# Optimization experiments

Hardware: AMD Instinct MI355X
Metric: run time of the kernel (lower is better)

The kernel has to match this reference:

```python
import jax, jax.numpy as jnp
import numpy as np

E_DIM = 64
N_EMBED = 8192

def setup_inputs() -> dict:
    key = jax.random.key(0)
    k1, k2 = jax.random.split(key)
    x = jax.random.normal(k1, (16, E_DIM, 32, 32), dtype=jnp.float32)   # [B, e_dim, H, W]
    embed = jax.random.normal(k2, (E_DIM, N_EMBED), dtype=jnp.float32)  # codebook [e_dim, n_embed]
    return {"x": x, "embed": embed}

def reference(x, embed):
    e_dim, n_embed = embed.shape
    # NCHW -> NHWC
    xp = jnp.transpose(x, (0, 2, 3, 1))              # [B, H, W, e_dim]
    flat = xp.reshape(-1, e_dim)                     # [N, e_dim]
    # squared-distance expansion: ||f||^2 - 2 f.E + ||e||^2  -> [N, n_embed]
    distance = (jnp.sum(flat * flat, axis=1, keepdims=True)
                - 2.0 * flat @ embed
                + jnp.sum(embed * embed, axis=0, keepdims=True))
    embed_idx = jnp.argmax(-distance, axis=1)        # [N] nearest code ids
    embed_idx = embed_idx.reshape(xp.shape[:-1])     # [B, H, W]
    # gather codes: embedding table is embed.T -> [n_embed, e_dim]
    quantize = jnp.take(embed.T, embed_idx, axis=0)  # [B, H, W, e_dim]
    return quantize
```

## Files before the change

kernel.cpp:

```cpp
#include <hip/hip_runtime.h>


typedef __attribute__((ext_vector_type(8))) __bf16 bf16x8;
typedef __attribute__((ext_vector_type(4))) float f32x4;
typedef unsigned int u32;
typedef unsigned long long u64;

union frag_cast { f32x4 f; bf16x8 b; };
__device__ __forceinline__ bf16x8 as_bf16x8(f32x4 v) { frag_cast u; u.f = v; return u.b; }

#define N_ROWS  16384
#define E_DIM   64
#define N_EMBED 8192
#define NCHUNK  16
#define COLS_PER_BLOCK (N_EMBED / NCHUNK)
#define N_ST (COLS_PER_BLOCK / 64)
#define ROWS_PER_BLOCK 512
#define N_ROWBLK (N_ROWS / ROWS_PER_BLOCK)
#define NT 8
#define MARGIN_THR 2e-3f

#define WS_AH   0u
#define WS_AL   (2u << 20)
#define WS_B    (4u << 20)
#define WS_ET   (6u << 20)
#define WS_BIAS (8u << 20)
#define WS_CNT  (WS_BIAS + (32u << 10))
#define WS_PB1  (WS_CNT + (4u << 10))
#define WS_PI1  (WS_PB1 + (1u << 20))
#define WS_PB2  (WS_PI1 + (1u << 20))

__device__ __forceinline__ u32 f32_key(float s) {
    u32 u = __float_as_uint(s);
    return (u & 0x80000000u) ? ~u : (u | 0x80000000u);
}

__device__ __forceinline__ void async16(const void* g, void* l) {
    __builtin_amdgcn_global_load_lds(
        (const __attribute__((address_space(1))) void*)g,
        (__attribute__((address_space(3))) void*)l, 16, 0, 0);
}

__global__ __launch_bounds__(256) void prep(
        const float* __restrict__ x, const float* __restrict__ embed, char* ws) {
    __shared__ float tile[64][65];
    __bf16* Ah = (__bf16*)(ws + WS_AH);
    __bf16* Al = (__bf16*)(ws + WS_AL);
    float*  eT = (float*)(ws + WS_ET);
    float*  bias = (float*)(ws + WS_BIAS);
    const int t = threadIdx.x;
    const int blk = blockIdx.x;

    if (blk < 256) {
        const int b = blk >> 4, p0 = (blk & 15) * 64;
        {
            const int c = t >> 2, seg = (t & 3) * 16;
            const float* src = x + b * 65536 + c * 1024 + p0 + seg;
#pragma unroll
            for (int i = 0; i < 16; ++i) tile[c][seg + i] = src[i];
        }
        __syncthreads();
        const int p = t >> 2, cq = (t & 3) * 16;
        const long row = b * 1024 + p0 + p;
        bf16x8 vh0, vh1, vl0, vl1;
#pragma unroll
        for (int i = 0; i < 16; ++i) {
            float f = tile[cq + i][p];
            __bf16 h = (__bf16)f;
            __bf16 l = (__bf16)(f - (float)h);
            if (i < 8) { vh0[i] = h; vl0[i] = l; }
            else       { vh1[i - 8] = h; vl1[i - 8] = l; }
        }
        *(bf16x8*)(Ah + row * 64 + cq) = vh0;
        *(bf16x8*)(Ah + row * 64 + cq + 8) = vh1;
        *(bf16x8*)(Al + row * 64 + cq) = vl0;
        *(bf16x8*)(Al + row * 64 + cq + 8) = vl1;
    } else {
        const int g = blk - 256;
        const int jbase = g * 64;
        char* Bg = ws + WS_B + (size_t)g * 16384;
        {
            const int c = t >> 2, seg = (t & 3) * 16;
            const float* src = embed + c * N_EMBED + jbase + seg;
#pragma unroll
            for (int i = 0; i < 16; ++i) tile[c][seg + i] = src[i];
        }
        __syncthreads();
        if (t < 64) {
            float s = 0.f;
#pragma unroll
            for (int c = 0; c < 64; ++c) { float v = tile[c][t]; s = fmaf(v, v, s); }
            bias[jbase + t] = -0.5f * s;
        }
        const int jl = t >> 2, cq = (t & 3) * 16;
        bf16x8 vh0, vh1, vl0, vl1;
#pragma unroll
        for (int i = 0; i < 16; ++i) {
            float f = tile[cq + i][jl];
            eT[(long)(jbase + jl) * 64 + cq + i] = f;
            __bf16 h = (__bf16)f;
            __bf16 l = (__bf16)(f - (float)h);
            if (i < 8) { vh0[i] = h; vl0[i] = l; }
            else       { vh1[i - 8] = h; vl1[i - 8] = l; }
        }
        const int k0 = (cq >> 3), sw = jl & 7;
        __bf16* hi = (__bf16*)Bg + jl * 64;
        __bf16* lo = (__bf16*)(Bg + 8192) + jl * 64;
        *(bf16x8*)(hi + ((k0 ^ sw) * 8))       = vh0;
        *(bf16x8*)(hi + (((k0 + 1) ^ sw) * 8)) = vh1;
        *(bf16x8*)(lo + ((k0 ^ sw) * 8))       = vl0;
        *(bf16x8*)(lo + (((k0 + 1) ^ sw) * 8)) = vl1;
    }
}

__global__ __launch_bounds__(256, 2) void qdist(const char* __restrict__ ws_c, char* __restrict__ ws) {
    __shared__ __align__(16) char smem[2][16384];
    const __bf16* Ah = (const __bf16*)(ws_c + WS_AH);
    const __bf16* Al = (const __bf16*)(ws_c + WS_AL);
    const char* Bws = ws_c + WS_B;
    const float* biasg = (const float*)(ws_c + WS_BIAS);
    float* pb1 = (float*)(ws + WS_PB1);
    int*   pi1 = (int*)(ws + WS_PI1);
    float* pb2 = (float*)(ws + WS_PB2);

    const int t = threadIdx.x;
    const int wv = t >> 6, lane = t & 63, ln = lane & 15, q = lane >> 4;
    const int rb = blockIdx.x >> 4, chunk = blockIdx.x & 15;
    const int row0 = rb * ROWS_PER_BLOCK;
    const int col0 = chunk * COLS_PER_BLOCK;
    const int g0 = col0 >> 6;

    f32x4 pfh[NT][2], pfl[NT][2];
#pragma unroll
    for (int nt = 0; nt < NT; ++nt) {
        long row = row0 + wv * 128 + nt * 16 + ln;
        long base = row * 64 + q * 8;
        pfh[nt][0] = *(const f32x4*)(Ah + base);
        pfh[nt][1] = *(const f32x4*)(Ah + base + 32);
        pfl[nt][0] = *(const f32x4*)(Al + base);
        pfl[nt][1] = *(const f32x4*)(Al + base + 32);
    }
    asm volatile("" :
        "+v"(pfh[0][0]), "+v"(pfh[0][1]), "+v"(pfh[1][0]), "+v"(pfh[1][1]),
        "+v"(pfh[2][0]), "+v"(pfh[2][1]), "+v"(pfh[3][0]), "+v"(pfh[3][1]),
        "+v"(pfh[4][0]), "+v"(pfh[4][1]), "+v"(pfh[5][0]), "+v"(pfh[5][1]),
        "+v"(pfh[6][0]), "+v"(pfh[6][1]), "+v"(pfh[7][0]), "+v"(pfh[7][1]));
    asm volatile("" :
        "+v"(pfl[0][0]), "+v"(pfl[0][1]), "+v"(pfl[1][0]), "+v"(pfl[1][1]),
        "+v"(pfl[2][0]), "+v"(pfl[2][1]), "+v"(pfl[3][0]), "+v"(pfl[3][1]),
        "+v"(pfl[4][0]), "+v"(pfl[4][1]), "+v"(pfl[5][0]), "+v"(pfl[5][1]),
        "+v"(pfl[6][0]), "+v"(pfl[6][1]), "+v"(pfl[7][0]), "+v"(pfl[7][1]));

    float b1[NT], b2[NT]; int iq[NT];
#pragma unroll
    for (int k = 0; k < NT; ++k) { b1[k] = -3.4e38f; b2[k] = -3.4e38f; iq[k] = 0; }

    const int s7 = ln & 7;
    const int rdbase = ln * 128 + ((q ^ s7) << 4);

    auto issue = [&](int st) {
        const char* src = Bws + (size_t)(g0 + st) * 16384;
        char* dst = smem[st & 1];
#pragma unroll
        for (int s = 0; s < 4; ++s)
            async16(src + s * 4096 + wv * 1024 + lane * 16,
                    dst + s * 4096 + wv * 1024);
    };

    issue(0);
    for (int st = 0; st < N_ST; ++st) {
        __syncthreads();
        if (st + 1 < N_ST) issue(st + 1);
        const char* buf = smem[st & 1];
        __builtin_amdgcn_s_setprio(1);
#pragma unroll
        for (int ct = 0; ct < 4; ++ct) {
            const int boff = ct * 2048 + rdbase;
            bf16x8 ah0 = *(const bf16x8*)(buf + boff);
            bf16x8 ah1 = *(const bf16x8*)(buf + (boff ^ 64));
            bf16x8 al0 = *(const bf16x8*)(buf + 8192 + boff);
            bf16x8 al1 = *(const bf16x8*)(buf + 8192 + (boff ^ 64));
            const int cbase = col0 + st * 64 + ct * 16;
            f32x4 bv = *(const f32x4*)(biasg + cbase + q * 4);
            const int jq = cbase + q * 4;
#pragma unroll
            for (int nt = 0; nt < NT; ++nt) {
                f32x4 acc = __builtin_amdgcn_mfma_f32_16x16x32_bf16(al0, as_bf16x8(pfh[nt][0]), bv, 0, 0, 0);
                acc = __builtin_amdgcn_mfma_f32_16x16x32_bf16(al1, as_bf16x8(pfh[nt][1]), acc, 0, 0, 0);
                acc = __builtin_amdgcn_mfma_f32_16x16x32_bf16(ah0, as_bf16x8(pfl[nt][0]), acc, 0, 0, 0);
                acc = __builtin_amdgcn_mfma_f32_16x16x32_bf16(ah1, as_bf16x8(pfl[nt][1]), acc, 0, 0, 0);
                acc = __builtin_amdgcn_mfma_f32_16x16x32_bf16(ah0, as_bf16x8(pfh[nt][0]), acc, 0, 0, 0);
                acc = __builtin_amdgcn_mfma_f32_16x16x32_bf16(ah1, as_bf16x8(pfh[nt][1]), acc, 0, 0, 0);
                float mx = fmaxf(fmaxf(acc[0], acc[1]), fmaxf(acc[2], acc[3]));
                b2[nt] = fmaxf(b2[nt], fminf(b1[nt], mx));
                bool gt = mx > b1[nt];
                b1[nt] = fmaxf(b1[nt], mx);
                iq[nt] = gt ? jq : iq[nt];
            }
        }
        __builtin_amdgcn_s_setprio(0);
    }

#pragma unroll
    for (int m = 16; m < 64; m <<= 1) {
#pragma unroll
        for (int nt = 0; nt < NT; ++nt) {
            float o1 = __shfl_xor(b1[nt], m);
            int   oi = __shfl_xor(iq[nt], m);
            float o2 = __shfl_xor(b2[nt], m);
            b2[nt] = fmaxf(fmaxf(fminf(b1[nt], o1), o2), b2[nt]);
            bool take = (o1 > b1[nt]) || (o1 == b1[nt] && oi < iq[nt]);
            if (take) { b1[nt] = o1; iq[nt] = oi; }
        }
    }
    if (q == 0) {
#pragma unroll
        for (int nt = 0; nt < NT; ++nt) {
            int pixel = row0 + wv * 128 + nt * 16 + ln;
            int o = chunk * N_ROWS + pixel;
            pb1[o] = b1[nt];
            pi1[o] = iq[nt];
            pb2[o] = b2[nt];
        }
    }
}

__global__ __launch_bounds__(256) void reduce_rows(const float* __restrict__ x, char* ws,
                                                   float* __restrict__ out) {
    const float* pb1 = (const float*)(ws + WS_PB1);
    const int*   pi1 = (const int*)(ws + WS_PI1);
    const float* pb2 = (const float*)(ws + WS_PB2);
    const float* eT = (const float*)(ws + WS_ET);
    const float* bias = (const float*)(ws + WS_BIAS);
    const int t = threadIdx.x;
    const int lane = t & 63, wv = t >> 6;
    const int row = (blockIdx.x * 256 + t) >> 2;
    const int sub = t & 3;

    float m1 = -3.4e38f, m2 = -3.4e38f; int mi = 0;
#pragma unroll
    for (int k = 0; k < 4; ++k) {
        const int ch = sub * 4 + k;
        float o1 = pb1[ch * N_ROWS + row];
        int   oi = pi1[ch * N_ROWS + row];
        float o2 = pb2[ch * N_ROWS + row];
        m2 = fmaxf(fmaxf(fminf(m1, o1), o2), m2);
        if (o1 > m1 || (o1 == m1 && oi < mi)) { m1 = o1; mi = oi; }
    }
#pragma unroll
    for (int m = 1; m < 4; m <<= 1) {
        float o1 = __shfl_xor(m1, m);
        int   oi = __shfl_xor(mi, m);
        float o2 = __shfl_xor(m2, m);
        m2 = fmaxf(fmaxf(fminf(m1, o1), o2), m2);
        bool take = (o1 > m1) || (o1 == m1 && oi < mi);
        if (take) { m1 = o1; mi = oi; }
    }

    const bool flagged = (m1 - m2 < MARGIN_THR);
    if (!flagged) {
        const float* xb = x + (row >> 10) * 65536 + (row & 1023);
        const int j = mi + sub;
        const f32x4* ecd = (const f32x4*)(eT + (size_t)j * 64);
        float s = bias[j];
#pragma unroll
        for (int v = 0; v < 16; ++v) {
            f32x4 ev = ecd[v];
            s = fmaf(xb[(v * 4 + 0) * 1024], ev[0], s);
            s = fmaf(xb[(v * 4 + 1) * 1024], ev[1], s);
            s = fmaf(xb[(v * 4 + 2) * 1024], ev[2], s);
            s = fmaf(xb[(v * 4 + 3) * 1024], ev[3], s);
        }
        float best = s; int bj = j;
#pragma unroll
        for (int m = 1; m < 4; m <<= 1) {
            float os = __shfl_xor(best, m);
            int   oj = __shfl_xor(bj, m);
            bool take = (os > best) || (os == best && oj < bj);
            if (take) { best = os; bj = oj; }
        }
        const f32x4* src = (const f32x4*)(eT + (size_t)bj * 64);
        f32x4* dst = (f32x4*)(out + (size_t)row * 64);
#pragma unroll
        for (int v = 0; v < 4; ++v) dst[v * 4 + sub] = src[v * 4 + sub];
    }

    u64 bal = __ballot(flagged);
    const int wrow0 = blockIdx.x * 64 + wv * 16;
    while (bal) {
        const int b = __ffsll(bal) - 1;
        const int rw = b >> 2;
        bal &= ~(0xFull << (rw * 4));
        const int r = wrow0 + rw;
        const float rb1 = __shfl(m1, rw * 4);
        const float cutoff = rb1 - 2.0f * MARGIN_THR;

        float xv = x[(r >> 10) * 65536 + lane * 1024 + (r & 1023)];
        float xr[64];
#pragma unroll
        for (int c = 0; c < 64; ++c) xr[c] = __shfl(xv, c);

        u64 bestk = 0ull;
        for (int ch = 0; ch < NCHUNK; ++ch) {
            if (pb1[ch * N_ROWS + r] < cutoff) continue;
#pragma unroll
            for (int k = 0; k < 8; ++k) {
                const int j = ch * 512 + lane * 8 + k;
                const f32x4* ecd = (const f32x4*)(eT + (size_t)j * 64);
                f32x4 a0 = {0.f, 0.f, 0.f, 0.f}, a1 = a0, a2 = a0, a3 = a0;
#pragma unroll
                for (int v = 0; v < 4; ++v) {
                    f32x4 e0 = ecd[v * 4 + 0], e1 = ecd[v * 4 + 1];
                    f32x4 e2 = ecd[v * 4 + 2], e3 = ecd[v * 4 + 3];
#pragma unroll
                    for (int kk = 0; kk < 4; ++kk) {
                        a0[kk] = fmaf(xr[v * 16 + kk],      e0[kk], a0[kk]);
                        a1[kk] = fmaf(xr[v * 16 + 4 + kk],  e1[kk], a1[kk]);
                        a2[kk] = fmaf(xr[v * 16 + 8 + kk],  e2[kk], a2[kk]);
                        a3[kk] = fmaf(xr[v * 16 + 12 + kk], e3[kk], a3[kk]);
                    }
                }
                f32x4 a01 = a0 + a1, a23 = a2 + a3;
                f32x4 as = a01 + a23;
                float s = bias[j] + ((as[0] + as[1]) + (as[2] + as[3]));
                u64 key = ((u64)f32_key(s) << 32) | (u32)(~(u32)j);
                bestk = (key > bestk) ? key : bestk;
            }
        }
#pragma unroll
        for (int m = 1; m < 64; m <<= 1) {
            u64 o = __shfl_xor(bestk, m);
            bestk = (o > bestk) ? o : bestk;
        }
        const int idx = (int)(~(u32)(bestk & 0xffffffffull));
        out[(size_t)r * 64 + lane] = eT[(size_t)idx * 64 + lane];
    }
}

extern "C" void kernel_launch(void* const* d_in, const int* in_sizes, int n_in,
                              void* d_out, int out_size, void* d_ws, size_t ws_size,
                              hipStream_t stream) {
    const float* x     = (const float*)d_in[0];
    const float* embed = (const float*)d_in[1];
    float* out = (float*)d_out;
    char* ws = (char*)d_ws;

    prep<<<384, 256, 0, stream>>>(x, embed, ws);
    qdist<<<N_ROWBLK * NCHUNK, 256, 0, stream>>>(ws, ws);
    reduce_rows<<<256, 256, 0, stream>>>(x, ws, out);
}
```

Before: 130.2 us.

## Switch distance GEMM to single-pass fp16 with norm-based rigorous rescoring margin

```diff
diff --git a/kernel.cpp b/kernel.cpp
--- a/kernel.cpp
+++ b/kernel.cpp
@@ -1,13 +1,11 @@
 #include <hip/hip_runtime.h>
 
 
-typedef __attribute__((ext_vector_type(8))) __bf16 bf16x8;
+typedef _Float16 f16;
+typedef __attribute__((ext_vector_type(8))) _Float16 f16x8;
 typedef __attribute__((ext_vector_type(4))) float f32x4;
 typedef unsigned int u32;
 typedef unsigned long long u64;
-
-union frag_cast { f32x4 f; bf16x8 b; };
-__device__ __forceinline__ bf16x8 as_bf16x8(f32x4 v) { frag_cast u; u.f = v; return u.b; }
 
 #define N_ROWS  16384
 #define E_DIM   64
@@ -18,17 +16,16 @@
 #define ROWS_PER_BLOCK 512
 #define N_ROWBLK (N_ROWS / ROWS_PER_BLOCK)
 #define NT 8
-#define MARGIN_THR 2e-3f
 
 #define WS_AH   0u
-#define WS_AL   (2u << 20)
-#define WS_B    (4u << 20)
-#define WS_ET   (6u << 20)
-#define WS_BIAS (8u << 20)
-#define WS_CNT  (WS_BIAS + (32u << 10))
-#define WS_PB1  (WS_CNT + (4u << 10))
-#define WS_PI1  (WS_PB1 + (1u << 20))
-#define WS_PB2  (WS_PI1 + (1u << 20))
+#define WS_B    (2u << 20)
+#define WS_ET   (3u << 20)
+#define WS_BIAS (5u << 20)
+#define WS_GN   (WS_BIAS + (32u << 10))
+#define WS_F2   (WS_BIAS + (36u << 10))
+#define WS_PB1  (6u << 20)
+#define WS_PI1  (7u << 20)
+#define WS_PB2  (8u << 20)
 
 __device__ __forceinline__ u32 f32_key(float s) {
     u32 u = __float_as_uint(s);
@@ -44,10 +41,11 @@
 __global__ __launch_bounds__(256) void prep(
         const float* __restrict__ x, const float* __restrict__ embed, char* ws) {
     __shared__ float tile[64][65];
-    __bf16* Ah = (__bf16*)(ws + WS_AH);
-    __bf16* Al = (__bf16*)(ws + WS_AL);
-    float*  eT = (float*)(ws + WS_ET);
-    float*  bias = (float*)(ws + WS_BIAS);
+    f16* Ah = (f16*)(ws + WS_AH);
+    float* eT = (float*)(ws + WS_ET);
+    float* bias = (float*)(ws + WS_BIAS);
+    float* gn = (float*)(ws + WS_GN);
+    float* f2g = (float*)(ws + WS_F2);
     const int t = threadIdx.x;
     const int blk = blockIdx.x;
 
@@ -62,23 +60,24 @@
         __syncthreads();
         const int p = t >> 2, cq = (t & 3) * 16;
         const long row = b * 1024 + p0 + p;
-        bf16x8 vh0, vh1, vl0, vl1;
+        f16x8 v0, v1;
+        float sq = 0.f;
 #pragma unroll
         for (int i = 0; i < 16; ++i) {
             float f = tile[cq + i][p];
-            __bf16 h = (__bf16)f;
-            __bf16 l = (__bf16)(f - (float)h);
-            if (i < 8) { vh0[i] = h; vl0[i] = l; }
-            else       { vh1[i - 8] = h; vl1[i - 8] = l; }
-        }
-        *(bf16x8*)(Ah + row * 64 + cq) = vh0;
-        *(bf16x8*)(Ah + row * 64 + cq + 8) = vh1;
-        *(bf16x8*)(Al + row * 64 + cq) = vl0;
-        *(bf16x8*)(Al + row * 64 + cq + 8) = vl1;
+            sq = fmaf(f, f, sq);
+            if (i < 8) v0[i] = (f16)f;
+            else       v1[i - 8] = (f16)f;
+        }
+        sq += __shfl_xor(sq, 1);
+        sq += __shfl_xor(sq, 2);
+        if ((t & 3) == 0) f2g[row] = sq;
+        *(f16x8*)(Ah + row * 64 + cq) = v0;
+        *(f16x8*)(Ah + row * 64 + cq + 8) = v1;
     } else {
         const int g = blk - 256;
         const int jbase = g * 64;
-        char* Bg = ws + WS_B + (size_t)g * 16384;
+        f16* Bg = (f16*)(ws + WS_B) + (size_t)g * 4096;
         {
             const int c = t >> 2, seg = (t & 3) * 16;
             const float* src = embed + c * N_EMBED + jbase + seg;
@@ -91,32 +90,31 @@
 #pragma unroll
             for (int c = 0; c < 64; ++c) { float v = tile[c][t]; s = fmaf(v, v, s); }
             bias[jbase + t] = -0.5f * s;
+            float m = s;
+#pragma unroll
+            for (int off = 1; off < 64; off <<= 1) m = fmaxf(m, __shfl_xor(m, off));
+            if (t == 0) gn[g] = m;
         }
         const int jl = t >> 2, cq = (t & 3) * 16;
-        bf16x8 vh0, vh1, vl0, vl1;
+        f16x8 v0, v1;
 #pragma unroll
         for (int i = 0; i < 16; ++i) {
             float f = tile[cq + i][jl];
             eT[(long)(jbase + jl) * 64 + cq + i] = f;
-            __bf16 h = (__bf16)f;
-            __bf16 l = (__bf16)(f - (float)h);
-            if (i < 8) { vh0[i] = h; vl0[i] = l; }
-            else       { vh1[i - 8] = h; vl1[i - 8] = l; }
+            if (i < 8) v0[i] = (f16)f;
+            else       v1[i - 8] = (f16)f;
         }
         const int k0 = (cq >> 3), sw = jl & 7;
-        __bf16* hi = (__bf16*)Bg + jl * 64;
-        __bf16* lo = (__bf16*)(Bg + 8192) + jl * 64;
-        *(bf16x8*)(hi + ((k0 ^ sw) * 8))       = vh0;
-        *(bf16x8*)(hi + (((k0 + 1) ^ sw) * 8)) = vh1;
-        *(bf16x8*)(lo + ((k0 ^ sw) * 8))       = vl0;
-        *(bf16x8*)(lo + (((k0 + 1) ^ sw) * 8)) = vl1;
+        f16* hi = Bg + jl * 64;
+        *(f16x8*)(hi + ((k0 ^ sw) * 8))       = v0;
+        *(f16x8*)(hi + (((k0 + 1) ^ sw) * 8)) = v1;
     }
 }
 
 __global__ __launch_bounds__(256, 2) void qdist(const char* __restrict__ ws_c, char* __restrict__ ws) {
-    __shared__ __align__(16) char smem[2][16384];
-    const __bf16* Ah = (const __bf16*)(ws_c + WS_AH);
-    const __bf16* Al = (const __bf16*)(ws_c + WS_AL);
+    __shared__ __align__(16) char smem[2][8192];
+    __shared__ __align__(16) float biasLds[512];
+    const f16* Ah = (const f16*)(ws_c + WS_AH);
     const char* Bws = ws_c + WS_B;
     const float* biasg = (const float*)(ws_c + WS_BIAS);
     float* pb1 = (float*)(ws + WS_PB1);
@@ -130,26 +128,19 @@
     const int col0 = chunk * COLS_PER_BLOCK;
     const int g0 = col0 >> 6;
 
-    f32x4 pfh[NT][2], pfl[NT][2];
+    f16x8 pf[NT][2];
 #pragma unroll
     for (int nt = 0; nt < NT; ++nt) {
         long row = row0 + wv * 128 + nt * 16 + ln;
         long base = row * 64 + q * 8;
-        pfh[nt][0] = *(const f32x4*)(Ah + base);
-        pfh[nt][1] = *(const f32x4*)(Ah + base + 32);
-        pfl[nt][0] = *(const f32x4*)(Al + base);
-        pfl[nt][1] = *(const f32x4*)(Al + base + 32);
+        pf[nt][0] = *(const f16x8*)(Ah + base);
+        pf[nt][1] = *(const f16x8*)(Ah + base + 32);
     }
     asm volatile("" :
-        "+v"(pfh[0][0]), "+v"(pfh[0][1]), "+v"(pfh[1][0]), "+v"(pfh[1][1]),
-        "+v"(pfh[2][0]), "+v"(pfh[2][1]), "+v"(pfh[3][0]), "+v"(pfh[3][1]),
-        "+v"(pfh[4][0]), "+v"(pfh[4][1]), "+v"(pfh[5][0]), "+v"(pfh[5][1]),
-        "+v"(pfh[6][0]), "+v"(pfh[6][1]), "+v"(pfh[7][0]), "+v"(pfh[7][1]));
-    asm volatile("" :
-        "+v"(pfl[0][0]), "+v"(pfl[0][1]), "+v"(pfl[1][0]), "+v"(pfl[1][1]),
-        "+v"(pfl[2][0]), "+v"(pfl[2][1]), "+v"(pfl[3][0]), "+v"(pfl[3][1]),
-        "+v"(pfl[4][0]), "+v"(pfl[4][1]), "+v"(pfl[5][0]), "+v"(pfl[5][1]),
-        "+v"(pfl[6][0]), "+v"(pfl[6][1]), "+v"(pfl[7][0]), "+v"(pfl[7][1]));
+        "+v"(pf[0][0]), "+v"(pf[0][1]), "+v"(pf[1][0]), "+v"(pf[1][1]),
+        "+v"(pf[2][0]), "+v"(pf[2][1]), "+v"(pf[3][0]), "+v"(pf[3][1]),
+        "+v"(pf[4][0]), "+v"(pf[4][1]), "+v"(pf[5][0]), "+v"(pf[5][1]),
+        "+v"(pf[6][0]), "+v"(pf[6][1]), "+v"(pf[7][0]), "+v"(pf[7][1]));
 
     float b1[NT], b2[NT]; int iq[NT];
 #pragma unroll
@@ -159,14 +150,17 @@
     const int rdbase = ln * 128 + ((q ^ s7) << 4);
 
     auto issue = [&](int st) {
-        const char* src = Bws + (size_t)(g0 + st) * 16384;
+        const char* src = Bws + (size_t)(g0 + st) * 8192;
         char* dst = smem[st & 1];
 #pragma unroll
-        for (int s = 0; s < 4; ++s)
+        for (int s = 0; s < 2; ++s)
             async16(src + s * 4096 + wv * 1024 + lane * 16,
                     dst + s * 4096 + wv * 1024);
     };
 
+    if (t < 128)
+        async16((const char*)(biasg + col0) + t * 16,
+                (char*)biasLds + (t >> 6) * 1024);
     issue(0);
     for (int st = 0; st < N_ST; ++st) {
         __syncthreads();
@@ -176,21 +170,14 @@
 #pragma unroll
         for (int ct = 0; ct < 4; ++ct) {
             const int boff = ct * 2048 + rdbase;
-            bf16x8 ah0 = *(const bf16x8*)(buf + boff);
-            bf16x8 ah1 = *(const bf16x8*)(buf + (boff ^ 64));
-            bf16x8 al0 = *(const bf16x8*)(buf + 8192 + boff);
-            bf16x8 al1 = *(const bf16x8*)(buf + 8192 + (boff ^ 64));
-            const int cbase = col0 + st * 64 + ct * 16;
-            f32x4 bv = *(const f32x4*)(biasg + cbase + q * 4);
-            const int jq = cbase + q * 4;
+            f16x8 ah0 = *(const f16x8*)(buf + boff);
+            f16x8 ah1 = *(const f16x8*)(buf + (boff ^ 64));
+            f32x4 bv = *(const f32x4*)(biasLds + st * 64 + ct * 16 + q * 4);
+            const int jq = col0 + st * 64 + ct * 16 + q * 4;
 #pragma unroll
             for (int nt = 0; nt < NT; ++nt) {
-                f32x4 acc = __builtin_amdgcn_mfma_f32_16x16x32_bf16(al0, as_bf16x8(pfh[nt][0]), bv, 0, 0, 0);
-                acc = __builtin_amdgcn_mfma_f32_16x16x32_bf16(al1, as_bf16x8(pfh[nt][1]), acc, 0, 0, 0);
-                acc = __builtin_amdgcn_mfma_f32_16x16x32_bf16(ah0, as_bf16x8(pfl[nt][0]), acc, 0, 0, 0);
-                acc = __builtin_amdgcn_mfma_f32_16x16x32_bf16(ah1, as_bf16x8(pfl[nt][1]), acc, 0, 0, 0);
-                acc = __builtin_amdgcn_mfma_f32_16x16x32_bf16(ah0, as_bf16x8(pfh[nt][0]), acc, 0, 0, 0);
-                acc = __builtin_amdgcn_mfma_f32_16x16x32_bf16(ah1, as_bf16x8(pfh[nt][1]), acc, 0, 0, 0);
+                f32x4 acc = __builtin_amdgcn_mfma_f32_16x16x32_f16(ah0, pf[nt][0], bv, 0, 0, 0);
+                acc = __builtin_amdgcn_mfma_f32_16x16x32_f16(ah1, pf[nt][1], acc, 0, 0, 0);
                 float mx = fmaxf(fmaxf(acc[0], acc[1]), fmaxf(acc[2], acc[3]));
                 b2[nt] = fmaxf(b2[nt], fminf(b1[nt], mx));
                 bool gt = mx > b1[nt];
@@ -232,23 +219,19 @@
     const float* pb2 = (const float*)(ws + WS_PB2);
     const float* eT = (const float*)(ws + WS_ET);
     const float* bias = (const float*)(ws + WS_BIAS);
+    const float* gn = (const float*)(ws + WS_GN);
+    const float* f2g = (const float*)(ws + WS_F2);
     const int t = threadIdx.x;
     const int lane = t & 63, wv = t >> 6;
-    const int row = (blockIdx.x * 256 + t) >> 2;
-    const int sub = t & 3;
-
-    float m1 = -3.4e38f, m2 = -3.4e38f; int mi = 0;
-#pragma unroll
-    for (int k = 0; k < 4; ++k) {
-        const int ch = sub * 4 + k;
-        float o1 = pb1[ch * N_ROWS + row];
-        int   oi = pi1[ch * N_ROWS + row];
-        float o2 = pb2[ch * N_ROWS + row];
-        m2 = fmaxf(fmaxf(fminf(m1, o1), o2), m2);
-        if (o1 > m1 || (o1 == m1 && oi < mi)) { m1 = o1; mi = oi; }
-    }
-#pragma unroll
-    for (int m = 1; m < 4; m <<= 1) {
+    const int sub = t & 15;
+    const int rw = (t & 63) >> 4;
+    const int row = blockIdx.x * 16 + wv * 4 + rw;
+
+    float m1 = pb1[sub * N_ROWS + row];
+    int   mi = pi1[sub * N_ROWS + row];
+    float m2 = pb2[sub * N_ROWS + row];
+#pragma unroll
+    for (int m = 1; m < 16; m <<= 1) {
         float o1 = __shfl_xor(m1, m);
         int   oi = __shfl_xor(mi, m);
         float o2 = __shfl_xor(m2, m);
@@ -257,20 +240,33 @@
         if (take) { m1 = o1; mi = oi; }
     }
 
-    const bool flagged = (m1 - m2 < MARGIN_THR);
+    f32x4 g0v = ((const f32x4*)gn)[sub * 2];
+    f32x4 g1v = ((const f32x4*)gn)[sub * 2 + 1];
+    float e2 = fmaxf(fmaxf(fmaxf(g0v[0], g0v[1]), fmaxf(g0v[2], g0v[3])),
+                     fmaxf(fmaxf(g1v[0], g1v[1]), fmaxf(g1v[2], g1v[3])));
+#pragma unroll
+    for (int m = 1; m < 16; m <<= 1) e2 = fmaxf(e2, __shfl_xor(e2, m));
+    const float f2 = f2g[row];
+    const float M = 1.01f * ldexpf(sqrtf(f2) * sqrtf(e2), -9) + 4e-3f;
+
+    const bool flagged = (m1 - m2 < M);
     if (!flagged) {
         const float* xb = x + (row >> 10) * 65536 + (row & 1023);
-        const int j = mi + sub;
-        const f32x4* ecd = (const f32x4*)(eT + (size_t)j * 64);
-        float s = bias[j];
-#pragma unroll
-        for (int v = 0; v < 16; ++v) {
+        const int j = mi + (sub & 3);
+        const int h = sub >> 2;
+        const f32x4* ecd = (const f32x4*)(eT + (size_t)j * 64 + h * 16);
+        float s = (h == 0) ? bias[j] : 0.f;
+#pragma unroll
+        for (int v = 0; v < 4; ++v) {
             f32x4 ev = ecd[v];
-            s = fmaf(xb[(v * 4 + 0) * 1024], ev[0], s);
-            s = fmaf(xb[(v * 4 + 1) * 1024], ev[1], s);
-            s = fmaf(xb[(v * 4 + 2) * 1024], ev[2], s);
-            s = fmaf(xb[(v * 4 + 3) * 1024], ev[3], s);
-        }
+            const int c0 = h * 16 + v * 4;
+            s = fmaf(xb[(c0 + 0) * 1024], ev[0], s);
+            s = fmaf(xb[(c0 + 1) * 1024], ev[1], s);
+            s = fmaf(xb[(c0 + 2) * 1024], ev[2], s);
+            s = fmaf(xb[(c0 + 3) * 1024], ev[3], s);
+        }
+        s += __shfl_xor(s, 4);
+        s += __shfl_xor(s, 8);
         float best = s; int bj = j;
 #pragma unroll
         for (int m = 1; m < 4; m <<= 1) {
@@ -279,21 +275,20 @@
             bool take = (os > best) || (os == best && oj < bj);
             if (take) { best = os; bj = oj; }
         }
-        const f32x4* src = (const f32x4*)(eT + (size_t)bj * 64);
-        f32x4* dst = (f32x4*)(out + (size_t)row * 64);
-#pragma unroll
-        for (int v = 0; v < 4; ++v) dst[v * 4 + sub] = src[v * 4 + sub];
+        ((f32x4*)(out + (size_t)row * 64))[sub] =
+            ((const f32x4*)(eT + (size_t)bj * 64))[sub];
     }
 
     u64 bal = __ballot(flagged);
-    const int wrow0 = blockIdx.x * 64 + wv * 16;
+    const int wrow0 = blockIdx.x * 16 + wv * 4;
     while (bal) {
         const int b = __ffsll(bal) - 1;
-        const int rw = b >> 2;
-        bal &= ~(0xFull << (rw * 4));
-        const int r = wrow0 + rw;
-        const float rb1 = __shfl(m1, rw * 4);
-        const float cutoff = rb1 - 2.0f * MARGIN_THR;
+        const int rr = b >> 4;
+        bal &= ~(0xFFFFull << (rr * 16));
+        const int r = wrow0 + rr;
+        const float rb1 = __shfl(m1, rr * 16);
+        const float rM  = __shfl(M,  rr * 16);
+        const float cutoff = rb1 - rM;
 
         float xv = x[(r >> 10) * 65536 + lane * 1024 + (r & 1023)];
         float xr[64];
@@ -311,12 +306,12 @@
 #pragma unroll
                 for (int v = 0; v < 4; ++v) {
                     f32x4 e0 = ecd[v * 4 + 0], e1 = ecd[v * 4 + 1];
-                    f32x4 e2 = ecd[v * 4 + 2], e3 = ecd[v * 4 + 3];
+                    f32x4 e2v = ecd[v * 4 + 2], e3 = ecd[v * 4 + 3];
 #pragma unroll
                     for (int kk = 0; kk < 4; ++kk) {
                         a0[kk] = fmaf(xr[v * 16 + kk],      e0[kk], a0[kk]);
                         a1[kk] = fmaf(xr[v * 16 + 4 + kk],  e1[kk], a1[kk]);
-                        a2[kk] = fmaf(xr[v * 16 + 8 + kk],  e2[kk], a2[kk]);
+                        a2[kk] = fmaf(xr[v * 16 + 8 + kk],  e2v[kk], a2[kk]);
                         a3[kk] = fmaf(xr[v * 16 + 12 + kk], e3[kk], a3[kk]);
                     }
                 }
@@ -347,5 +342,5 @@
 
     prep<<<384, 256, 0, stream>>>(x, embed, ws);
     qdist<<<N_ROWBLK * NCHUNK, 256, 0, stream>>>(ws, ws);
-    reduce_rows<<<256, 256, 0, stream>>>(x, ws, out);
-}
+    reduce_rows<<<N_ROWS / 16, 256, 0, stream>>>(x, ws, out);
+}
```

New measurement: 198.2 us. +52.2%, slower.
